# Optimization experiments

Measured on AMD Instinct MI355X. Metric: run time of the kernel, lower is better.

Reference implementation:

```python
import jax, jax.numpy as jnp
import numpy as np

B, T, E, H, R = 128, 64, 2048, 1024, 8  # batch, context_window, utter_hidden*2, user_dim, max_roles


def _gru_params(key, in_dim, hid):
    k1, k2, k3, k4 = jax.random.split(key, 4)
    s = 1.0 / np.sqrt(hid)
    return (jax.random.uniform(k1, (3 * hid, in_dim), jnp.float32, -s, s),
            jax.random.uniform(k2, (3 * hid, hid), jnp.float32, -s, s),
            jax.random.uniform(k3, (3 * hid,), jnp.float32, -s, s),
            jax.random.uniform(k4, (3 * hid,), jnp.float32, -s, s))


def setup_inputs() -> dict:
    key = jax.random.key(0)
    ks = jax.random.split(key, 8)
    encoder_hiddens = jax.random.normal(ks[0], (B, T, E), jnp.float32)
    spk = jax.random.randint(ks[1], (B, T), 0, R)
    adr = (spk + jax.random.randint(ks[2], (B, T), 1, R)) % R  # guarantee adr != spk
    dig_users = jnp.stack([spk, adr], axis=-1).astype(jnp.int32)  # [B,T,2]
    ws_ih, ws_hh, ws_bih, ws_bhh = _gru_params(ks[3], E + H, H)  # GRUS: input=[enc; adr_state]
    wa_ih, wa_hh, wa_bih, wa_bhh = _gru_params(ks[4], E + H, H)  # GRUA: input=[enc; spk_state]
    wo_ih, wo_hh, wo_bih, wo_bhh = _gru_params(ks[5], E, H)      # GRUO: input=enc
    return dict(encoder_hiddens=encoder_hiddens, dig_users=dig_users,
                ws_ih=ws_ih, ws_hh=ws_hh, ws_bih=ws_bih, ws_bhh=ws_bhh,
                wa_ih=wa_ih, wa_hh=wa_hh, wa_bih=wa_bih, wa_bhh=wa_bhh,
                wo_ih=wo_ih, wo_hh=wo_hh, wo_bih=wo_bih, wo_bhh=wo_bhh)


def _gru_cell(x, h, w_ih, w_hh, b_ih, b_hh):
    # standard torch.nn.GRUCell math; x: [..., in_dim], h: [..., H]
    gi = x @ w_ih.T + b_ih
    gh = h @ w_hh.T + b_hh
    ir, iz, ig = jnp.split(gi, 3, axis=-1)
    hr, hz, hg = jnp.split(gh, 3, axis=-1)
    r = jax.nn.sigmoid(ir + hr)
    z = jax.nn.sigmoid(iz + hz)
    n = jnp.tanh(ig + r * hg)
    return (1.0 - z) * n + z * h


def reference(encoder_hiddens, dig_users, ws_ih, ws_hh, ws_bih, ws_bhh,
              wa_ih, wa_hh, wa_bih, wa_bhh, wo_ih, wo_hh, wo_bih, wo_bhh):
    bidx = jnp.arange(B)
    roles = jnp.arange(R)

    def step(A, xs):
        enc_t, spk_t, adr_t = xs  # [B,E], [B], [B]
        # others: ascending role indices excluding spk and adr -> [B, R-2]
        is_other = (roles[None, :] != spk_t[:, None]) & (roles[None, :] != adr_t[:, None])
        others = jnp.argsort(jnp.logical_not(is_other).astype(jnp.int32), axis=-1, stable=True)[:, : R - 2]
        # gather current role states (all from pre-update A, as in the original)
        spk_v = A[bidx, spk_t]                    # [B,H]
        adr_v = A[bidx, adr_t]                    # [B,H]
        oth_v = A[bidx[:, None], others]          # [B,R-2,H]
        new_spk = _gru_cell(jnp.concatenate([enc_t, adr_v], -1), spk_v, ws_ih, ws_hh, ws_bih, ws_bhh)
        new_adr = _gru_cell(jnp.concatenate([enc_t, spk_v], -1), adr_v, wa_ih, wa_hh, wa_bih, wa_bhh)
        enc_b = jnp.broadcast_to(enc_t[:, None, :], (B, R - 2, E))
        new_oth = _gru_cell(enc_b, oth_v, wo_ih, wo_hh, wo_bih, wo_bhh)
        # scatter back (spk, adr, others indices are disjoint per batch row)
        A = A.at[bidx, spk_t].set(new_spk)
        A = A.at[bidx, adr_t].set(new_adr)
        A = A.at[bidx[:, None], others].set(new_oth)
        return A, None

    A0 = jnp.zeros((B, R, H), jnp.float32)
    xs = (jnp.swapaxes(encoder_hiddens, 0, 1),  # [T,B,E]
          jnp.swapaxes(dig_users[..., 0], 0, 1),
          jnp.swapaxes(dig_users[..., 1], 0, 1))
    A, _ = jax.lax.scan(step, A0, xs)
    return A
```

## Files before the change

### kernel.cpp

```cpp
#include <hip/hip_runtime.h>
#include <math.h>
#include <stdint.h>

static constexpr int B_ = 128;
static constexpr int T_ = 64;
static constexpr int E_ = 2048;
static constexpr int H_ = 1024;
static constexpr int R_ = 8;
static constexpr int H3_ = 3 * H_;

typedef unsigned short u16;
typedef __attribute__((ext_vector_type(8))) __bf16 bf16x8;
typedef __attribute__((ext_vector_type(4))) float f32x4;

__device__ __forceinline__ u16 f2bf(float f) {
    uint32_t x = __float_as_uint(f);
    x += 0x7fffu + ((x >> 16) & 1u);
    return (u16)(x >> 16);
}
__device__ __forceinline__ float bf2f(u16 u) {
    return __uint_as_float(((uint32_t)u) << 16);
}

__device__ __forceinline__ void async_cp16(const u16* g, u16* l) {
    auto* g1 = (const __attribute__((address_space(1))) u16*)g;
    auto* l3 = (__attribute__((address_space(3))) u16*)(uintptr_t)l;
    __builtin_amdgcn_global_load_lds((const __attribute__((address_space(1))) void*)g1,
                                     (__attribute__((address_space(3))) void*)l3,
                                     16, 0, 0);
}

__global__ __launch_bounds__(256) void zero_kernel(float* __restrict__ p, int n) {
    int i = blockIdx.x * 256 + threadIdx.x;
    if (i < n) p[i] = 0.0f;
}

__global__ __launch_bounds__(256) void conv_bf(
    const float* __restrict__ src, int src_ld, int col0, int cols,
    u16* __restrict__ dst, int total4)
{
    int i4 = blockIdx.x * 256 + threadIdx.x;
    if (i4 >= total4) return;
    int i = i4 * 4;
    int r = i / cols, c = i - r * cols;
    const float4 v = *(const float4*)(src + (size_t)r * src_ld + col0 + c);
    ushort4 o;
    o.x = f2bf(v.x); o.y = f2bf(v.y); o.z = f2bf(v.z); o.w = f2bf(v.w);
    *(ushort4*)(dst + i) = o;
}

__global__ __launch_bounds__(256) void mfma_p1f(
    const u16* __restrict__ X, int t0, int tcshift,
    const u16* __restrict__ W1,
    const float* __restrict__ bs, const float* __restrict__ ba,
    const float* __restrict__ bo,
    u16* __restrict__ GI, size_t GI_elems)
{
    __shared__ u16 As[2][128 * 32];
    __shared__ u16 Bs[2][128 * 32];
    __shared__ int rowoff[128];
    const int tid = threadIdx.x;
    const int which = blockIdx.x / 24;
    const int n0 = (blockIdx.x % 24) * 128;
    const int m0 = blockIdx.y * 128;
    const int tcmask = (1 << tcshift) - 1;

    const u16* W = W1 + (size_t)which * H3_ * E_;
    const float* bias = (which == 0) ? bs : (which == 1) ? ba : bo;
    u16* C = GI + (size_t)which * GI_elems;

    if (tid < 128) {
        int m = m0 + tid;
        rowoff[tid] = ((m >> tcshift) * T_ + t0 + (m & tcmask)) * E_;
    }
    __syncthreads();

    const int lane = tid & 63;
    const int wm = ((tid >> 6) & 1) * 64;
    const int wn = (tid >> 7) * 64;
    const int fr = lane & 15;
    const int kq = (lane >> 4) * 8;
    const int wbase = (tid & 192) * 8;

    f32x4 acc[4][4] = {};

    auto stage = [&](int buf, int k0) {
#pragma unroll
        for (int p = 0; p < 2; ++p) {
            int c = p * 256 + tid;
            int row = c >> 2, kc = (c & 3) * 8;
            async_cp16(X + rowoff[row] + k0 + kc, &As[buf][p * 2048 + wbase]);
            async_cp16(W + (size_t)(n0 + row) * E_ + k0 + kc, &Bs[buf][p * 2048 + wbase]);
        }
    };
    auto compute = [&](int buf) {
        bf16x8 a[4], b[4];
#pragma unroll
        for (int i = 0; i < 4; ++i) {
            a[i] = *(const bf16x8*)&As[buf][(wm + i * 16 + fr) * 32 + kq];
            b[i] = *(const bf16x8*)&Bs[buf][(wn + i * 16 + fr) * 32 + kq];
        }
#pragma unroll
        for (int mt = 0; mt < 4; ++mt)
#pragma unroll
            for (int nt = 0; nt < 4; ++nt)
                acc[mt][nt] = __builtin_amdgcn_mfma_f32_16x16x32_bf16(
                    a[mt], b[nt], acc[mt][nt], 0, 0, 0);
    };

    stage(0, 0);
    __syncthreads();
    int cur = 0;
    for (int k0 = 32; k0 < E_; k0 += 32) {
        stage(cur ^ 1, k0);
        compute(cur);
        __syncthreads();
        cur ^= 1;
    }
    compute(cur);

#pragma unroll
    for (int mt = 0; mt < 4; ++mt)
#pragma unroll
        for (int nt = 0; nt < 4; ++nt) {
            int n = n0 + wn + nt * 16 + fr;
            float bv = bias[n];
#pragma unroll
            for (int i = 0; i < 4; ++i) {
                int m = m0 + wm + mt * 16 + (lane >> 4) * 4 + i;
                C[(size_t)m * H3_ + n] = f2bf(acc[mt][nt][i] + bv);
            }
        }
}

__global__ __launch_bounds__(256) void mfma_step(
    const u16* __restrict__ Abf, const int* __restrict__ dig, int t,
    const u16* __restrict__ Whsi, const u16* __restrict__ Whs,
    const u16* __restrict__ Whai, const u16* __restrict__ Wha,
    const u16* __restrict__ Who, float* __restrict__ G)
{
    __shared__ u16 As[2][64 * 32];
    __shared__ u16 Bs[2][128 * 32];
    __shared__ int rowoff[64];
    const int tid = threadIdx.x;
    const int n0 = blockIdx.x * 128;
    const int row0 = blockIdx.y * 64;

    const u16* W;
    if      (row0 < 128) W = Whsi;
    else if (row0 < 256) W = Whs;
    else if (row0 < 384) W = Whai;
    else if (row0 < 512) W = Wha;
    else                 W = Who;

    if (tid < 64) {
        int mo = row0 + tid;
        int b, role;
        if (mo < 512) {
            b = mo & 127;
            int kind = mo >> 7;
            int spk = dig[(b * T_ + t) * 2 + 0];
            int adr = dig[(b * T_ + t) * 2 + 1];
            role = (kind == 0 || kind == 3) ? adr : spk;
        } else {
            int o = mo - 512;
            b = o / 6;
            int j = o - b * 6;
            int spk = dig[(b * T_ + t) * 2 + 0];
            int adr = dig[(b * T_ + t) * 2 + 1];
            int cnt = 0; role = 0;
            for (int r = 0; r < R_; ++r) {
                if (r != spk && r != adr) {
                    if (cnt == j) { role = r; break; }
                    ++cnt;
                }
            }
        }
        rowoff[tid] = (b * R_ + role) * H_;
    }
    __syncthreads();

    const int lane = tid & 63;
    const int wid = tid >> 6;
    const int wm = (wid & 1) * 32;
    const int wn = (wid >> 1) * 64;
    const int fr = lane & 15;
    const int kq = (lane >> 4) * 8;
    const int wbase = (tid & 192) * 8;

    f32x4 acc[2][4] = {};

    auto stage = [&](int buf, int k0) {
        {
            int row = tid >> 2, kc = (tid & 3) * 8;
            async_cp16(Abf + rowoff[row] + k0 + kc, &As[buf][wbase]);
        }
#pragma unroll
        for (int p = 0; p < 2; ++p) {
            int c = p * 256 + tid;
            int row = c >> 2, kc = (c & 3) * 8;
            async_cp16(W + (size_t)(n0 + row) * H_ + k0 + kc, &Bs[buf][p * 2048 + wbase]);
        }
    };
    auto compute = [&](int buf) {
        bf16x8 a[2], b[4];
#pragma unroll
        for (int i = 0; i < 2; ++i)
            a[i] = *(const bf16x8*)&As[buf][(wm + i * 16 + fr) * 32 + kq];
#pragma unroll
        for (int j = 0; j < 4; ++j)
            b[j] = *(const bf16x8*)&Bs[buf][(wn + j * 16 + fr) * 32 + kq];
#pragma unroll
        for (int mt = 0; mt < 2; ++mt)
#pragma unroll
            for (int nt = 0; nt < 4; ++nt)
                acc[mt][nt] = __builtin_amdgcn_mfma_f32_16x16x32_bf16(
                    a[mt], b[nt], acc[mt][nt], 0, 0, 0);
    };

    stage(0, 0);
    __syncthreads();
    int cur = 0;
    for (int k0 = 32; k0 < H_; k0 += 32) {
        stage(cur ^ 1, k0);
        compute(cur);
        __syncthreads();
        cur ^= 1;
    }
    compute(cur);

#pragma unroll
    for (int mt = 0; mt < 2; ++mt)
#pragma unroll
        for (int nt = 0; nt < 4; ++nt) {
            int n = n0 + wn + nt * 16 + fr;
#pragma unroll
            for (int i = 0; i < 4; ++i) {
                int mo = row0 + wm + mt * 16 + (lane >> 4) * 4 + i;
                G[(size_t)mo * H3_ + n] = acc[mt][nt][i];
            }
        }
}

__global__ __launch_bounds__(256) void gate_kernel(
    const float* __restrict__ Aold, float* __restrict__ Anew,
    u16* __restrict__ Abf,
    const int* __restrict__ dig, int t, int tloc, int Tc,
    const u16* __restrict__ GIX, const u16* __restrict__ GIA,
    const u16* __restrict__ GIO, const float* __restrict__ G,
    const float* __restrict__ ws_bhh, const float* __restrict__ wa_bhh,
    const float* __restrict__ wo_bhh)
{
    const int blk = blockIdx.x;
    const int b = blk >> 3, r = blk & 7;
    const int spk = dig[(b * T_ + t) * 2 + 0];
    const int adr = dig[(b * T_ + t) * 2 + 1];
    const size_t gi_row = (size_t)(b * Tc + tloc) * H3_;

    const u16* gi_pre;
    const float* gi_add;
    const float* gh;
    const float* bhh;
    if (r == spk) {
        gi_pre = GIX + gi_row;
        gi_add = G + (size_t)b * H3_;
        gh     = G + (size_t)(128 + b) * H3_;
        bhh    = ws_bhh;
    } else if (r == adr) {
        gi_pre = GIA + gi_row;
        gi_add = G + (size_t)(256 + b) * H3_;
        gh     = G + (size_t)(384 + b) * H3_;
        bhh    = wa_bhh;
    } else {
        int oidx = r - (spk < r ? 1 : 0) - (adr < r ? 1 : 0);
        gi_pre = GIO + gi_row;
        gi_add = nullptr;
        gh     = G + (size_t)(512 + b * 6 + oidx) * H3_;
        bhh    = wo_bhh;
    }

    const size_t hoff = (size_t)(b * R_ + r) * H_;
    for (int i = threadIdx.x; i < H_; i += 256) {
        float gir = bf2f(gi_pre[i]);
        float giz = bf2f(gi_pre[H_ + i]);
        float gin = bf2f(gi_pre[2 * H_ + i]);
        if (gi_add) {
            gir += gi_add[i];
            giz += gi_add[H_ + i];
            gin += gi_add[2 * H_ + i];
        }
        float ghr = gh[i]          + bhh[i];
        float ghz = gh[H_ + i]     + bhh[H_ + i];
        float ghn = gh[2 * H_ + i] + bhh[2 * H_ + i];

        float rg = 1.0f / (1.0f + __expf(-(gir + ghr)));
        float zg = 1.0f / (1.0f + __expf(-(giz + ghz)));
        float ng = tanhf(gin + rg * ghn);
        float h  = Aold[hoff + i];
        float o  = (1.0f - zg) * ng + zg * h;
        Anew[hoff + i] = o;
        Abf[hoff + i]  = f2bf(o);
    }
}

extern "C" void kernel_launch(void* const* d_in, const int* in_sizes, int n_in,
                              void* d_out, int out_size, void* d_ws, size_t ws_size,
                              hipStream_t stream) {
    const float* enc    = (const float*)d_in[0];
    const int*   dig    = (const int*)d_in[1];
    const float* ws_ih  = (const float*)d_in[2];
    const float* ws_hh  = (const float*)d_in[3];
    const float* ws_bih = (const float*)d_in[4];
    const float* ws_bhh = (const float*)d_in[5];
    const float* wa_ih  = (const float*)d_in[6];
    const float* wa_hh  = (const float*)d_in[7];
    const float* wa_bih = (const float*)d_in[8];
    const float* wa_bhh = (const float*)d_in[9];
    const float* wo_ih  = (const float*)d_in[10];
    const float* wo_hh  = (const float*)d_in[11];
    const float* wo_bih = (const float*)d_in[12];
    const float* wo_bhh = (const float*)d_in[13];

    float* A0 = (float*)d_out;

    char* p = (char*)d_ws;
    auto take = [&](size_t bytes) { char* q = p; p += (bytes + 255) & ~(size_t)255; return q; };
    u16*   enc_bf = (u16*)  take((size_t)B_ * T_ * E_ * 2);
    u16*   W1     = (u16*)  take((size_t)3 * H3_ * E_ * 2);
    u16*   W1s    = W1;
    u16*   W1a    = W1 + (size_t)H3_ * E_;
    u16*   W1o    = W1a + (size_t)H3_ * E_;
    u16*   Whsi   = (u16*)  take((size_t)H3_ * H_ * 2);
    u16*   Whai   = (u16*)  take((size_t)H3_ * H_ * 2);
    u16*   Whs    = (u16*)  take((size_t)H3_ * H_ * 2);
    u16*   Wha    = (u16*)  take((size_t)H3_ * H_ * 2);
    u16*   Who    = (u16*)  take((size_t)H3_ * H_ * 2);
    u16*   Abf    = (u16*)  take((size_t)B_ * R_ * H_ * 2);
    float* A1     = (float*)take((size_t)B_ * R_ * H_ * 4);
    float* G      = (float*)take((size_t)1280 * H3_ * 4);
    size_t fixed = (size_t)(p - (char*)d_ws);

    const size_t per_t = (size_t)3 * B_ * H3_ * 2;
    int Tc = 64;
    while (Tc > 1 && fixed + per_t * (size_t)Tc > ws_size) Tc >>= 1;
    int tcshift = 0;
    while ((1 << tcshift) < Tc) ++tcshift;
    const size_t GI_elems = (size_t)B_ * Tc * H3_;
    u16* GI  = (u16*)take(3 * GI_elems * 2);
    u16* GIX = GI;
    u16* GIA = GI + GI_elems;
    u16* GIO = GIA + GI_elems;

    dim3 blk(256);
    const size_t A_sz = (size_t)B_ * R_ * H_;

    zero_kernel<<<dim3((int)((A_sz + 255) / 256)), blk, 0, stream>>>(A0, (int)A_sz);
    zero_kernel<<<dim3((int)((A_sz / 2 + 255) / 256)), blk, 0, stream>>>((float*)Abf, (int)(A_sz / 2));

    {
        int t4;
        t4 = B_ * T_ * E_ / 4;
        conv_bf<<<dim3((t4 + 255) / 256), blk, 0, stream>>>(enc, E_, 0, E_, enc_bf, t4);
        t4 = H3_ * E_ / 4;
        conv_bf<<<dim3((t4 + 255) / 256), blk, 0, stream>>>(ws_ih, E_ + H_, 0, E_, W1s, t4);
        conv_bf<<<dim3((t4 + 255) / 256), blk, 0, stream>>>(wa_ih, E_ + H_, 0, E_, W1a, t4);
        conv_bf<<<dim3((t4 + 255) / 256), blk, 0, stream>>>(wo_ih, E_, 0, E_, W1o, t4);
        t4 = H3_ * H_ / 4;
        conv_bf<<<dim3((t4 + 255) / 256), blk, 0, stream>>>(ws_ih, E_ + H_, E_, H_, Whsi, t4);
        conv_bf<<<dim3((t4 + 255) / 256), blk, 0, stream>>>(wa_ih, E_ + H_, E_, H_, Whai, t4);
        conv_bf<<<dim3((t4 + 255) / 256), blk, 0, stream>>>(ws_hh, H_, 0, H_, Whs, t4);
        conv_bf<<<dim3((t4 + 255) / 256), blk, 0, stream>>>(wa_hh, H_, 0, H_, Wha, t4);
        conv_bf<<<dim3((t4 + 255) / 256), blk, 0, stream>>>(wo_hh, H_, 0, H_, Who, t4);
    }

    float* Aold = A0;
    float* Anew = A1;
    for (int t0 = 0; t0 < T_; t0 += Tc) {
        dim3 g1(72, (B_ * Tc) / 128);
        mfma_p1f<<<g1, blk, 0, stream>>>(enc_bf, t0, tcshift, W1,
                                         ws_bih, wa_bih, wo_bih, GI, GI_elems);

        for (int t = t0; t < t0 + Tc; ++t) {
            mfma_step<<<dim3(24, 20), blk, 0, stream>>>(
                Abf, dig, t, Whsi, Whs, Whai, Wha, Who, G);
            gate_kernel<<<dim3(B_ * R_), blk, 0, stream>>>(
                Aold, Anew, Abf, dig, t, t - t0, Tc, GIX, GIA, GIO, G,
                ws_bhh, wa_bhh, wo_bhh);
            float* tmp = Aold; Aold = Anew; Anew = tmp;
        }
    }
}
```

Baseline: 2.482 ms.

## Deepen K tile to 64 with XOR-swizzled LDS and halve step-GEMM N tile

Both GEMM kernels now stage 64-wide K slices instead of 32 and store them in LDS with an XOR swizzle on 16-byte chunks, which avoids bank conflicts on fragment reads and halves the number of barrier iterations. The input-projection kernel computes row offsets inline instead of through a shared rowoff table, dropping one sync. The per-step recurrent GEMM uses 64-wide N tiles, so it launches twice as many blocks (48x20) for more CU occupancy, at the cost of less reuse of each A tile.

```diff
diff --git a/kernel.cpp b/kernel.cpp
--- a/kernel.cpp
+++ b/kernel.cpp
@@ -29,6 +29,7 @@
                                      (__attribute__((address_space(3))) void*)l3,
                                      16, 0, 0);
 }
+
 
 __global__ __launch_bounds__(256) void zero_kernel(float* __restrict__ p, int n) {
     int i = blockIdx.x * 256 + threadIdx.x;
@@ -56,9 +57,8 @@
     const float* __restrict__ bo,
     u16* __restrict__ GI, size_t GI_elems)
 {
-    __shared__ u16 As[2][128 * 32];
-    __shared__ u16 Bs[2][128 * 32];
-    __shared__ int rowoff[128];
+    __shared__ u16 As[2][128 * 64];
+    __shared__ u16 Bs[2][128 * 64];
     const int tid = threadIdx.x;
     const int which = blockIdx.x / 24;
     const int n0 = (blockIdx.x % 24) * 128;
@@ -69,49 +69,54 @@
     const float* bias = (which == 0) ? bs : (which == 1) ? ba : bo;
     u16* C = GI + (size_t)which * GI_elems;
 
-    if (tid < 128) {
-        int m = m0 + tid;
-        rowoff[tid] = ((m >> tcshift) * T_ + t0 + (m & tcmask)) * E_;
-    }
-    __syncthreads();
-
     const int lane = tid & 63;
     const int wm = ((tid >> 6) & 1) * 64;
     const int wn = (tid >> 7) * 64;
     const int fr = lane & 15;
     const int kq = (lane >> 4) * 8;
-    const int wbase = (tid & 192) * 8;
+    const int ldsbase = (tid & 192) * 8;
+
+    const int srow = tid >> 3;
+    const int sce  = (((tid & 7) * 16) ^ ((srow & 7) << 4)) >> 1;
 
     f32x4 acc[4][4] = {};
 
     auto stage = [&](int buf, int k0) {
 #pragma unroll
-        for (int p = 0; p < 2; ++p) {
-            int c = p * 256 + tid;
-            int row = c >> 2, kc = (c & 3) * 8;
-            async_cp16(X + rowoff[row] + k0 + kc, &As[buf][p * 2048 + wbase]);
-            async_cp16(W + (size_t)(n0 + row) * E_ + k0 + kc, &Bs[buf][p * 2048 + wbase]);
+        for (int p = 0; p < 4; ++p) {
+            int mrow = m0 + p * 32 + srow;
+            int ro = ((mrow >> tcshift) * T_ + t0 + (mrow & tcmask)) * E_;
+            async_cp16(X + ro + k0 + sce, &As[buf][p * 2048 + ldsbase]);
+            int nrow = n0 + p * 32 + srow;
+            async_cp16(W + (size_t)nrow * E_ + k0 + sce, &Bs[buf][p * 2048 + ldsbase]);
         }
     };
     auto compute = [&](int buf) {
-        bf16x8 a[4], b[4];
-#pragma unroll
-        for (int i = 0; i < 4; ++i) {
-            a[i] = *(const bf16x8*)&As[buf][(wm + i * 16 + fr) * 32 + kq];
-            b[i] = *(const bf16x8*)&Bs[buf][(wn + i * 16 + fr) * 32 + kq];
-        }
-#pragma unroll
-        for (int mt = 0; mt < 4; ++mt)
-#pragma unroll
-            for (int nt = 0; nt < 4; ++nt)
-                acc[mt][nt] = __builtin_amdgcn_mfma_f32_16x16x32_bf16(
-                    a[mt], b[nt], acc[mt][nt], 0, 0, 0);
+#pragma unroll
+        for (int kk = 0; kk < 2; ++kk) {
+            bf16x8 a[4], b[4];
+#pragma unroll
+            for (int i = 0; i < 4; ++i) {
+                int ra = wm + i * 16 + fr;
+                int oa = (ra * 128 + kk * 64 + kq * 2) ^ ((ra & 7) << 4);
+                a[i] = *(const bf16x8*)((const char*)&As[buf][0] + oa);
+                int rb = wn + i * 16 + fr;
+                int ob = (rb * 128 + kk * 64 + kq * 2) ^ ((rb & 7) << 4);
+                b[i] = *(const bf16x8*)((const char*)&Bs[buf][0] + ob);
+            }
+#pragma unroll
+            for (int mt = 0; mt < 4; ++mt)
+#pragma unroll
+                for (int nt = 0; nt < 4; ++nt)
+                    acc[mt][nt] = __builtin_amdgcn_mfma_f32_16x16x32_bf16(
+                        a[mt], b[nt], acc[mt][nt], 0, 0, 0);
+        }
     };
 
     stage(0, 0);
     __syncthreads();
     int cur = 0;
-    for (int k0 = 32; k0 < E_; k0 += 32) {
+    for (int k0 = 64; k0 < E_; k0 += 64) {
         stage(cur ^ 1, k0);
         compute(cur);
         __syncthreads();
@@ -139,11 +144,11 @@
     const u16* __restrict__ Whai, const u16* __restrict__ Wha,
     const u16* __restrict__ Who, float* __restrict__ G)
 {
-    __shared__ u16 As[2][64 * 32];
-    __shared__ u16 Bs[2][128 * 32];
+    __shared__ u16 As[2][64 * 64];
+    __shared__ u16 Bs[2][64 * 64];
     __shared__ int rowoff[64];
     const int tid = threadIdx.x;
-    const int n0 = blockIdx.x * 128;
+    const int n0 = blockIdx.x * 64;
     const int row0 = blockIdx.y * 64;
 
     const u16* W;
@@ -183,45 +188,50 @@
     const int lane = tid & 63;
     const int wid = tid >> 6;
     const int wm = (wid & 1) * 32;
-    const int wn = (wid >> 1) * 64;
+    const int wn = (wid >> 1) * 32;
     const int fr = lane & 15;
     const int kq = (lane >> 4) * 8;
-    const int wbase = (tid & 192) * 8;
-
-    f32x4 acc[2][4] = {};
+    const int ldsbase = (tid & 192) * 8;
+
+    const int srow = tid >> 3;
+    const int sce  = (((tid & 7) * 16) ^ ((srow & 7) << 4)) >> 1;
+
+    f32x4 acc[2][2] = {};
 
     auto stage = [&](int buf, int k0) {
-        {
-            int row = tid >> 2, kc = (tid & 3) * 8;
-            async_cp16(Abf + rowoff[row] + k0 + kc, &As[buf][wbase]);
-        }
 #pragma unroll
         for (int p = 0; p < 2; ++p) {
-            int c = p * 256 + tid;
-            int row = c >> 2, kc = (c & 3) * 8;
-            async_cp16(W + (size_t)(n0 + row) * H_ + k0 + kc, &Bs[buf][p * 2048 + wbase]);
+            int r = p * 32 + srow;
+            async_cp16(Abf + rowoff[r] + k0 + sce, &As[buf][p * 2048 + ldsbase]);
+            async_cp16(W + (size_t)(n0 + r) * H_ + k0 + sce, &Bs[buf][p * 2048 + ldsbase]);
         }
     };
     auto compute = [&](int buf) {
-        bf16x8 a[2], b[4];
-#pragma unroll
-        for (int i = 0; i < 2; ++i)
-            a[i] = *(const bf16x8*)&As[buf][(wm + i * 16 + fr) * 32 + kq];
-#pragma unroll
-        for (int j = 0; j < 4; ++j)
-            b[j] = *(const bf16x8*)&Bs[buf][(wn + j * 16 + fr) * 32 + kq];
-#pragma unroll
-        for (int mt = 0; mt < 2; ++mt)
-#pragma unroll
-            for (int nt = 0; nt < 4; ++nt)
-                acc[mt][nt] = __builtin_amdgcn_mfma_f32_16x16x32_bf16(
-                    a[mt], b[nt], acc[mt][nt], 0, 0, 0);
+#pragma unroll
+        for (int kk = 0; kk < 2; ++kk) {
+            bf16x8 a[2], b[2];
+#pragma unroll
+            for (int i = 0; i < 2; ++i) {
+                int ra = wm + i * 16 + fr;
+                int oa = (ra * 128 + kk * 64 + kq * 2) ^ ((ra & 7) << 4);
+                a[i] = *(const bf16x8*)((const char*)&As[buf][0] + oa);
+                int rb = wn + i * 16 + fr;
+                int ob = (rb * 128 + kk * 64 + kq * 2) ^ ((rb & 7) << 4);
+                b[i] = *(const bf16x8*)((const char*)&Bs[buf][0] + ob);
+            }
+#pragma unroll
+            for (int mt = 0; mt < 2; ++mt)
+#pragma unroll
+                for (int nt = 0; nt < 2; ++nt)
+                    acc[mt][nt] = __builtin_amdgcn_mfma_f32_16x16x32_bf16(
+                        a[mt], b[nt], acc[mt][nt], 0, 0, 0);
+        }
     };
 
     stage(0, 0);
     __syncthreads();
     int cur = 0;
-    for (int k0 = 32; k0 < H_; k0 += 32) {
+    for (int k0 = 64; k0 < H_; k0 += 64) {
         stage(cur ^ 1, k0);
         compute(cur);
         __syncthreads();
@@ -232,7 +242,7 @@
 #pragma unroll
     for (int mt = 0; mt < 2; ++mt)
 #pragma unroll
-        for (int nt = 0; nt < 4; ++nt) {
+        for (int nt = 0; nt < 2; ++nt) {
             int n = n0 + wn + nt * 16 + fr;
 #pragma unroll
             for (int i = 0; i < 4; ++i) {
@@ -381,7 +391,7 @@
                                          ws_bih, wa_bih, wo_bih, GI, GI_elems);
 
         for (int t = t0; t < t0 + Tc; ++t) {
-            mfma_step<<<dim3(24, 20), blk, 0, stream>>>(
+            mfma_step<<<dim3(48, 20), blk, 0, stream>>>(
                 Abf, dig, t, Whsi, Whs, Whai, Wha, Who, G);
             gate_kernel<<<dim3(B_ * R_), blk, 0, stream>>>(
                 Aold, Anew, Abf, dig, t, t - t0, Tc, GIX, GIA, GIO, G,
```

New measurement: 2.168 ms. 1.15x faster.
